# Kernel optimization log

Measured on AMD Instinct MI355X. Metric: run time of the kernel, lower is better.

Reference implementation:

```python
import jax, jax.numpy as jnp
import numpy as np

ALPHA = 0.2   # LeakyReLU negative slope
RATIO = 0.5   # blend ratio between attention and structural similarity
KHOP = 3      # k-hop structural similarity depth
NEG_BIG = -9e15


def _build_adj(edge, n):
    # edge: [N, D] int neighbor indices; adj[i, edge[i, d]] = 1
    rows = jnp.broadcast_to(jnp.arange(n)[:, None], edge.shape)
    return jnp.zeros((n, n), jnp.float32).at[rows, edge].set(1.0)


def _structural_similarity(adj, khop):
    # Sum of adjacency powers A + A^2 + ... + A^khop (k-hop reachability counts).
    s = adj
    p = adj
    for _ in range(khop - 1):
        p = p @ adj
        s = s + p
    return s


def _per_graph(atom, edge, W, a):
    n = atom.shape[0]
    adj = _build_adj(edge, n)
    structure = jax.nn.softmax(_structural_similarity(adj, KHOP), axis=1)
    h = atom @ W                                   # [N, F]
    f = h.shape[1]
    # a_input[i,j] = concat(h_i, h_j); a_input @ a == (h @ a1)_i + (h @ a2)_j
    src = h @ a[:f, 0]                             # [N]
    dst = h @ a[f:, 0]                             # [N]
    e = jax.nn.leaky_relu(src[:, None] + dst[None, :], ALPHA)  # [N, N]
    att = jnp.where(adj > 0, e, NEG_BIG)
    att = jax.nn.softmax(att, axis=1)
    blended = RATIO * att + (1.0 - RATIO) * structure
    return jax.nn.elu(blended @ h)                 # [N, F]


def setup_inputs() -> dict:
    key = jax.random.key(0)
    k1, k2, k3, k4 = jax.random.split(key, 4)
    B, N, D, F_IN, F_OUT = 16, 1024, 8, 128, 64
    atoms = jax.random.normal(k1, (B, N, F_IN), dtype=jnp.float32)
    edges = jax.random.randint(k2, (B, N, D), 0, N, dtype=jnp.int64)
    W = jax.random.normal(k3, (F_IN, F_OUT), dtype=jnp.float32) * 0.1
    a = jax.random.normal(k4, (2 * F_OUT, 1), dtype=jnp.float32) * 0.1
    return {"atoms": atoms, "edges": edges, "W": W, "a": a}


def reference(atoms, edges, W, a):
    return jax.vmap(_per_graph, in_axes=(0, 0, None, None))(atoms, edges, W, a)
```

## Files before the change

### kernel.cpp

```cpp
#include <hip/hip_runtime.h>

#define NN 1024
#define DG 8
#define FO 64
#define FI 128
#define LALPHA 0.2f
#define BR 16
#define SBS 257
#define MTS 1032

typedef __attribute__((ext_vector_type(8))) short bf16x8;
typedef __attribute__((ext_vector_type(4))) float f32x4;

static __device__ __forceinline__ unsigned short f2bf(float x) {
  union { float f; unsigned u; } v; v.f = x;
  unsigned r = v.u + 0x7FFFu + ((v.u >> 16) & 1u);
  return (unsigned short)(r >> 16);
}
static __device__ __forceinline__ float bf2f(unsigned short h) {
  union { unsigned u; float f; } v; v.u = ((unsigned)h) << 16;
  return v.f;
}

__global__ __launch_bounds__(256) void k_uniq(const int* __restrict__ edges,
                                              int* __restrict__ uniq, int nrows) {
  int r = blockIdx.x * 256 + threadIdx.x;
  if (r >= nrows) return;
  int e[DG];
#pragma unroll
  for (int s = 0; s < DG; s++) e[s] = edges[r * DG + s];
#pragma unroll
  for (int s = 0; s < DG; s++) {
    int v = e[s];
    bool dup = false;
#pragma unroll
    for (int q = 0; q < DG; q++)
      if (q < s && e[q] == v) dup = true;
    uniq[r * DG + s] = dup ? -1 : v;
  }
}

__global__ __launch_bounds__(256) void k_h(const float* __restrict__ atoms,
                                           const float* __restrict__ W,
                                           const float* __restrict__ a,
                                           ushort* __restrict__ hT,
                                           float* __restrict__ srcv,
                                           float* __restrict__ dstv) {
  __shared__ __align__(16) ushort Ahi[64 * 136], Alo[64 * 136];
  __shared__ __align__(16) ushort Whi[64 * 136], Wlo[64 * 136];
  __shared__ float al[2 * FO];
  const int t = threadIdx.x, b = blockIdx.x;

  const float4* at4 = (const float4*)(atoms + (size_t)b * 64 * FI);
#pragma unroll
  for (int q = 0; q < 8; q++) {
    int idx = t + 256 * q;
    float4 v = at4[idx];
    int row = idx >> 5, c4 = (idx & 31) * 4;
    ushort h0 = f2bf(v.x), h1 = f2bf(v.y), h2 = f2bf(v.z), h3 = f2bf(v.w);
    ushort l0 = f2bf(v.x - bf2f(h0)), l1 = f2bf(v.y - bf2f(h1));
    ushort l2_ = f2bf(v.z - bf2f(h2)), l3 = f2bf(v.w - bf2f(h3));
    union { uint2 v; ushort u[4]; } ph, pl;
    ph.u[0] = h0; ph.u[1] = h1; ph.u[2] = h2; ph.u[3] = h3;
    pl.u[0] = l0; pl.u[1] = l1; pl.u[2] = l2_; pl.u[3] = l3;
    *(uint2*)&Ahi[row * 136 + c4] = ph.v;
    *(uint2*)&Alo[row * 136 + c4] = pl.v;
  }
  const float4* w4 = (const float4*)W;
#pragma unroll
  for (int q = 0; q < 8; q++) {
    int idx = t + 256 * q;
    float4 v = w4[idx];
    int c = idx >> 4, f0 = (idx & 15) * 4;
    float vv[4] = {v.x, v.y, v.z, v.w};
#pragma unroll
    for (int e = 0; e < 4; e++) {
      ushort hi = f2bf(vv[e]);
      Whi[(f0 + e) * 136 + c] = hi;
      Wlo[(f0 + e) * 136 + c] = f2bf(vv[e] - bf2f(hi));
    }
  }
  if (t < 2 * FO) al[t] = a[t];
  __syncthreads();

  const int w = t >> 6, lane = t & 63, quad = lane >> 4, l16 = lane & 15;
  f32x4 acc[4] = {{0.f, 0.f, 0.f, 0.f}, {0.f, 0.f, 0.f, 0.f},
                  {0.f, 0.f, 0.f, 0.f}, {0.f, 0.f, 0.f, 0.f}};
#pragma unroll
  for (int kc = 0; kc < 4; kc++) {
    int ko = kc * 32 + quad * 8;
    bf16x8 ahi = *(const bf16x8*)&Ahi[(w * 16 + l16) * 136 + ko];
    bf16x8 alo = *(const bf16x8*)&Alo[(w * 16 + l16) * 136 + ko];
#pragma unroll
    for (int ct = 0; ct < 4; ct++) {
      bf16x8 bhi = *(const bf16x8*)&Whi[(ct * 16 + l16) * 136 + ko];
      bf16x8 blo = *(const bf16x8*)&Wlo[(ct * 16 + l16) * 136 + ko];
      acc[ct] = __builtin_amdgcn_mfma_f32_16x16x32_bf16(ahi, bhi, acc[ct], 0, 0, 0);
      acc[ct] = __builtin_amdgcn_mfma_f32_16x16x32_bf16(ahi, blo, acc[ct], 0, 0, 0);
      acc[ct] = __builtin_amdgcn_mfma_f32_16x16x32_bf16(alo, bhi, acc[ct], 0, 0, 0);
    }
  }

  const int g = b >> 4;
  float ps[4] = {0.f, 0.f, 0.f, 0.f}, pd[4] = {0.f, 0.f, 0.f, 0.f};
#pragma unroll
  for (int ct = 0; ct < 4; ct++) {
    int f = ct * 16 + l16;
    float as_ = al[f], ad_ = al[FO + f];
#pragma unroll
    for (int r = 0; r < 4; r++) {
      float v = acc[ct][r];
      int rb = b * 64 + w * 16 + quad * 4 + r;
      int n = rb & (NN - 1);
      hT[((size_t)g * FO + f) * NN + n] = f2bf(v);
      ps[r] += v * as_;
      pd[r] += v * ad_;
    }
  }
#pragma unroll
  for (int off = 8; off > 0; off >>= 1)
#pragma unroll
    for (int r = 0; r < 4; r++) {
      ps[r] += __shfl_xor(ps[r], off);
      pd[r] += __shfl_xor(pd[r], off);
    }
  if (l16 == 0) {
#pragma unroll
    for (int r = 0; r < 4; r++) {
      int rb = b * 64 + w * 16 + quad * 4 + r;
      srcv[rb] = ps[r];
      dstv[rb] = pd[r];
    }
  }
}

__global__ __launch_bounds__(256) void k_fused(const int* __restrict__ uniq,
                                               const float* __restrict__ srcv,
                                               const float* __restrict__ dstv,
                                               const ushort* __restrict__ hT,
                                               float* __restrict__ out) {
  __shared__ unsigned Sb[BR * SBS];
  __shared__ __align__(16) ushort Mt[BR * MTS];
  __shared__ int n1[BR][DG];
  __shared__ float attw[BR][DG];
  __shared__ float zl[BR][16];
  __shared__ float Zr[BR];

  const int t = threadIdx.x, b = blockIdx.x;
  const int g = b >> 6, rbase = (b & 63) * BR;
  const int* __restrict__ Ug = uniq + (size_t)g * NN * DG;

  for (int i = t; i < BR * SBS; i += 256) Sb[i] = 0u;
  if (t < BR * DG) n1[t >> 3][t & 7] = Ug[(rbase + (t >> 3)) * DG + (t & 7)];
  __syncthreads();

  if (t < 128) {
    int r = t >> 3, s = t & 7;
    int j = n1[r][s];
    if (j >= 0) {
      atomicAdd(&Sb[r * SBS + (j >> 2)], 1u << ((j & 3) * 8));
      int4 k0 = *(const int4*)(Ug + j * DG);
      int4 k1 = *(const int4*)(Ug + j * DG + 4);
      int kk[8] = {k0.x, k0.y, k0.z, k0.w, k1.x, k1.y, k1.z, k1.w};
#pragma unroll
      for (int e = 0; e < 8; e++)
        if (kk[e] >= 0) atomicAdd(&Sb[r * SBS + (kk[e] >> 2)], 1u << ((kk[e] & 3) * 8));
    }
  } else if (t < 128 + BR) {
    int r = t - 128;
    float si = srcv[g * NN + rbase + r];
    float ev[DG];
    float m = -1e30f;
#pragma unroll
    for (int s = 0; s < DG; s++) {
      int j = n1[r][s];
      if (j >= 0) {
        float x = si + dstv[g * NN + j];
        x = x > 0.f ? x : LALPHA * x;
        ev[s] = x;
        m = fmaxf(m, x);
      } else ev[s] = -1e30f;
    }
    float sm = 0.f;
#pragma unroll
    for (int s = 0; s < DG; s++) {
      float e = (n1[r][s] >= 0) ? __expf(ev[s] - m) : 0.f;
      ev[s] = e;
      sm += e;
    }
    float inv = 1.f / sm;
#pragma unroll
    for (int s = 0; s < DG; s++) attw[r][s] = ev[s] * inv;
  }
#pragma unroll
  for (int q = 0; q < 4; q++) {
    int idx = t + 256 * q;
    int r = idx >> 6, e = idx & 63;
    int j = n1[r][e >> 3];
    if (j >= 0) {
      int k = Ug[j * DG + (e & 7)];
      if (k >= 0) {
        int4 m0 = *(const int4*)(Ug + k * DG);
        int4 m1 = *(const int4*)(Ug + k * DG + 4);
        int ll[8] = {m0.x, m0.y, m0.z, m0.w, m1.x, m1.y, m1.z, m1.w};
#pragma unroll
        for (int e2 = 0; e2 < 8; e2++)
          if (ll[e2] >= 0) atomicAdd(&Sb[r * SBS + (ll[e2] >> 2)], 1u << ((ll[e2] & 3) * 8));
      }
    }
  }
  __syncthreads();

  {
    int r = t & 15, u = t >> 4;
    float zp = 0.f;
#pragma unroll
    for (int q = 0; q < 16; q++) {
      unsigned sv = Sb[r * SBS + u * 16 + q];
      zp += __expf((float)(sv & 255u)) + __expf((float)((sv >> 8) & 255u)) +
            __expf((float)((sv >> 16) & 255u)) + __expf((float)(sv >> 24));
    }
    zl[r][u] = zp;
  }
  __syncthreads();
  if (t < BR) {
    float s = 0.f;
#pragma unroll
    for (int u = 0; u < 16; u++) s += zl[t][u];
    Zr[t] = s;
  }
  __syncthreads();

  {
    int r = t & 15, u = t >> 4;
    float hzi = 0.5f / Zr[r];
#pragma unroll
    for (int q = 0; q < 8; q++) {
      unsigned s0 = Sb[r * SBS + u * 16 + 2 * q];
      unsigned s1 = Sb[r * SBS + u * 16 + 2 * q + 1];
      union { uint4 v; ushort us[8]; } pk;
      pk.us[0] = f2bf(hzi * __expf((float)(s0 & 255u)));
      pk.us[1] = f2bf(hzi * __expf((float)((s0 >> 8) & 255u)));
      pk.us[2] = f2bf(hzi * __expf((float)((s0 >> 16) & 255u)));
      pk.us[3] = f2bf(hzi * __expf((float)(s0 >> 24)));
      pk.us[4] = f2bf(hzi * __expf((float)(s1 & 255u)));
      pk.us[5] = f2bf(hzi * __expf((float)((s1 >> 8) & 255u)));
      pk.us[6] = f2bf(hzi * __expf((float)((s1 >> 16) & 255u)));
      pk.us[7] = f2bf(hzi * __expf((float)(s1 >> 24)));
      *(uint4*)&Mt[r * MTS + u * 64 + q * 8] = pk.v;
    }
  }
  __syncthreads();
  if (t < 128) {
    int r = t >> 3, s = t & 7;
    int j = n1[r][s];
    if (j >= 0) {
      int adr = r * MTS + j;
      Mt[adr] = f2bf(bf2f(Mt[adr]) + 0.5f * attw[r][s]);
    }
  }
  __syncthreads();

  const int w = t >> 6, lane = t & 63, quad = lane >> 4, l16 = lane & 15;
  const ushort* __restrict__ hrow = hT + ((size_t)g * FO + w * 16 + l16) * NN;
  f32x4 acc = {0.f, 0.f, 0.f, 0.f};
#pragma unroll 4
  for (int ks = 0; ks < NN; ks += 32) {
    bf16x8 af = *(const bf16x8*)&Mt[l16 * MTS + ks + quad * 8];
    bf16x8 bf = *(const bf16x8*)(hrow + ks + quad * 8);
    acc = __builtin_amdgcn_mfma_f32_16x16x32_bf16(af, bf, acc, 0, 0, 0);
  }
#pragma unroll
  for (int r = 0; r < 4; r++) {
    int row = rbase + quad * 4 + r;
    float v = acc[r];
    v = v > 0.f ? v : __expf(v) - 1.f;
    out[((size_t)(g * NN + row)) * FO + w * 16 + l16] = v;
  }
}

extern "C" void kernel_launch(void* const* d_in, const int* in_sizes, int n_in,
                              void* d_out, int out_size, void* d_ws, size_t ws_size,
                              hipStream_t stream) {
  const float* atoms = (const float*)d_in[0];
  const int* edges = (const int*)d_in[1];
  const float* W = (const float*)d_in[2];
  const float* a = (const float*)d_in[3];
  float* out = (float*)d_out;

  const int nrows = in_sizes[0] / FI;
  const int ngraph = nrows / NN;

  ushort* hT = (ushort*)d_ws;
  float* srcv = (float*)(hT + (size_t)ngraph * FO * NN);
  float* dstv = srcv + nrows;
  int* uniq = (int*)(dstv + nrows);

  k_uniq<<<(nrows + 255) / 256, 256, 0, stream>>>(edges, uniq, nrows);
  k_h<<<nrows / 64, 256, 0, stream>>>(atoms, W, a, hT, srcv, dstv);
  k_fused<<<ngraph * (NN / BR), 256, 0, stream>>>(uniq, srcv, dstv, hT, out);
}
```

Before: 99.54 us.

## Merge uniq and h kernels into one prep kernel; defer softmax normalization

Folds the edge-dedup kernel into the h-projection kernel, cutting one launch. The new kernel uses 16-row blocks and loads atoms and W straight from global memory into MFMA operands, with no LDS staging. In the fused kernel the structural softmax normalization moves to the epilogue, which removes a barrier and a reduction pass. The attention weights are pre-scaled by Z so the final single scale stays correct. Risks: uncoalesced strided W loads repeated across many more blocks, and bf16 rounding of unnormalized exp values, which can reach e^255 and overflow.

```diff
diff --git a/kernel.cpp b/kernel.cpp
--- a/kernel.cpp
+++ b/kernel.cpp
@@ -22,115 +22,94 @@
   return v.f;
 }
 
-__global__ __launch_bounds__(256) void k_uniq(const int* __restrict__ edges,
-                                              int* __restrict__ uniq, int nrows) {
-  int r = blockIdx.x * 256 + threadIdx.x;
-  if (r >= nrows) return;
-  int e[DG];
-#pragma unroll
-  for (int s = 0; s < DG; s++) e[s] = edges[r * DG + s];
-#pragma unroll
-  for (int s = 0; s < DG; s++) {
-    int v = e[s];
-    bool dup = false;
-#pragma unroll
-    for (int q = 0; q < DG; q++)
-      if (q < s && e[q] == v) dup = true;
-    uniq[r * DG + s] = dup ? -1 : v;
-  }
-}
-
-__global__ __launch_bounds__(256) void k_h(const float* __restrict__ atoms,
-                                           const float* __restrict__ W,
-                                           const float* __restrict__ a,
-                                           ushort* __restrict__ hT,
-                                           float* __restrict__ srcv,
-                                           float* __restrict__ dstv) {
-  __shared__ __align__(16) ushort Ahi[64 * 136], Alo[64 * 136];
-  __shared__ __align__(16) ushort Whi[64 * 136], Wlo[64 * 136];
-  __shared__ float al[2 * FO];
+__global__ __launch_bounds__(256) void k_prep(const float* __restrict__ atoms,
+                                              const float* __restrict__ W,
+                                              const float* __restrict__ a,
+                                              const int* __restrict__ edges,
+                                              int* __restrict__ uniq,
+                                              ushort* __restrict__ hT,
+                                              float* __restrict__ srcv,
+                                              float* __restrict__ dstv) {
+  __shared__ float sp[16], dp[16];
   const int t = threadIdx.x, b = blockIdx.x;
-
-  const float4* at4 = (const float4*)(atoms + (size_t)b * 64 * FI);
-#pragma unroll
-  for (int q = 0; q < 8; q++) {
-    int idx = t + 256 * q;
-    float4 v = at4[idx];
-    int row = idx >> 5, c4 = (idx & 31) * 4;
-    ushort h0 = f2bf(v.x), h1 = f2bf(v.y), h2 = f2bf(v.z), h3 = f2bf(v.w);
-    ushort l0 = f2bf(v.x - bf2f(h0)), l1 = f2bf(v.y - bf2f(h1));
-    ushort l2_ = f2bf(v.z - bf2f(h2)), l3 = f2bf(v.w - bf2f(h3));
-    union { uint2 v; ushort u[4]; } ph, pl;
-    ph.u[0] = h0; ph.u[1] = h1; ph.u[2] = h2; ph.u[3] = h3;
-    pl.u[0] = l0; pl.u[1] = l1; pl.u[2] = l2_; pl.u[3] = l3;
-    *(uint2*)&Ahi[row * 136 + c4] = ph.v;
-    *(uint2*)&Alo[row * 136 + c4] = pl.v;
-  }
-  const float4* w4 = (const float4*)W;
-#pragma unroll
-  for (int q = 0; q < 8; q++) {
-    int idx = t + 256 * q;
-    float4 v = w4[idx];
-    int c = idx >> 4, f0 = (idx & 15) * 4;
-    float vv[4] = {v.x, v.y, v.z, v.w};
-#pragma unroll
-    for (int e = 0; e < 4; e++) {
-      ushort hi = f2bf(vv[e]);
-      Whi[(f0 + e) * 136 + c] = hi;
-      Wlo[(f0 + e) * 136 + c] = f2bf(vv[e] - bf2f(hi));
-    }
-  }
-  if (t < 2 * FO) al[t] = a[t];
-  __syncthreads();
+  const int g = b >> 6;
+  const int rbase = b * 16;
+
+  if (t < 16) {
+    sp[t] = 0.f; dp[t] = 0.f;
+    const int rr = rbase + t;
+    int e[DG];
+#pragma unroll
+    for (int s = 0; s < DG; s++) e[s] = edges[rr * DG + s];
+#pragma unroll
+    for (int s = 0; s < DG; s++) {
+      int v = e[s];
+      bool dup = false;
+#pragma unroll
+      for (int q = 0; q < DG; q++)
+        if (q < s && e[q] == v) dup = true;
+      uniq[rr * DG + s] = dup ? -1 : v;
+    }
+  }
 
   const int w = t >> 6, lane = t & 63, quad = lane >> 4, l16 = lane & 15;
-  f32x4 acc[4] = {{0.f, 0.f, 0.f, 0.f}, {0.f, 0.f, 0.f, 0.f},
-                  {0.f, 0.f, 0.f, 0.f}, {0.f, 0.f, 0.f, 0.f}};
+  const float* __restrict__ Ar = atoms + (size_t)(rbase + l16) * FI;
+  const float* __restrict__ Wc = W + w * 16 + l16;
+  f32x4 acc = {0.f, 0.f, 0.f, 0.f};
 #pragma unroll
   for (int kc = 0; kc < 4; kc++) {
-    int ko = kc * 32 + quad * 8;
-    bf16x8 ahi = *(const bf16x8*)&Ahi[(w * 16 + l16) * 136 + ko];
-    bf16x8 alo = *(const bf16x8*)&Alo[(w * 16 + l16) * 136 + ko];
-#pragma unroll
-    for (int ct = 0; ct < 4; ct++) {
-      bf16x8 bhi = *(const bf16x8*)&Whi[(ct * 16 + l16) * 136 + ko];
-      bf16x8 blo = *(const bf16x8*)&Wlo[(ct * 16 + l16) * 136 + ko];
-      acc[ct] = __builtin_amdgcn_mfma_f32_16x16x32_bf16(ahi, bhi, acc[ct], 0, 0, 0);
-      acc[ct] = __builtin_amdgcn_mfma_f32_16x16x32_bf16(ahi, blo, acc[ct], 0, 0, 0);
-      acc[ct] = __builtin_amdgcn_mfma_f32_16x16x32_bf16(alo, bhi, acc[ct], 0, 0, 0);
-    }
-  }
-
-  const int g = b >> 4;
-  float ps[4] = {0.f, 0.f, 0.f, 0.f}, pd[4] = {0.f, 0.f, 0.f, 0.f};
-#pragma unroll
-  for (int ct = 0; ct < 4; ct++) {
-    int f = ct * 16 + l16;
-    float as_ = al[f], ad_ = al[FO + f];
-#pragma unroll
-    for (int r = 0; r < 4; r++) {
-      float v = acc[ct][r];
-      int rb = b * 64 + w * 16 + quad * 4 + r;
-      int n = rb & (NN - 1);
-      hT[((size_t)g * FO + f) * NN + n] = f2bf(v);
-      ps[r] += v * as_;
-      pd[r] += v * ad_;
-    }
-  }
-#pragma unroll
-  for (int off = 8; off > 0; off >>= 1)
+    const int k0 = kc * 32 + quad * 8;
+    float4 a0 = *(const float4*)(Ar + k0);
+    float4 a1 = *(const float4*)(Ar + k0 + 4);
+    float av[8] = {a0.x, a0.y, a0.z, a0.w, a1.x, a1.y, a1.z, a1.w};
+    float wv[8];
+#pragma unroll
+    for (int e = 0; e < 8; e++) wv[e] = Wc[(k0 + e) * FO];
+    bf16x8 ahi, alo, bhi, blo;
+#pragma unroll
+    for (int e = 0; e < 8; e++) {
+      ushort h = f2bf(av[e]);
+      ahi[e] = (short)h;
+      alo[e] = (short)f2bf(av[e] - bf2f(h));
+      ushort g2 = f2bf(wv[e]);
+      bhi[e] = (short)g2;
+      blo[e] = (short)f2bf(wv[e] - bf2f(g2));
+    }
+    acc = __builtin_amdgcn_mfma_f32_16x16x32_bf16(ahi, bhi, acc, 0, 0, 0);
+    acc = __builtin_amdgcn_mfma_f32_16x16x32_bf16(ahi, blo, acc, 0, 0, 0);
+    acc = __builtin_amdgcn_mfma_f32_16x16x32_bf16(alo, bhi, acc, 0, 0, 0);
+  }
+
+  const int f = w * 16 + l16;
+  const float as_ = a[f], ad_ = a[FO + f];
+  float ps[4], pd[4];
+#pragma unroll
+  for (int r = 0; r < 4; r++) {
+    float v = acc[r];
+    int rb = rbase + quad * 4 + r;
+    hT[((size_t)g * FO + f) * NN + (rb & (NN - 1))] = f2bf(v);
+    ps[r] = v * as_;
+    pd[r] = v * ad_;
+  }
+#pragma unroll
+  for (int off = 1; off < 16; off <<= 1)
 #pragma unroll
     for (int r = 0; r < 4; r++) {
       ps[r] += __shfl_xor(ps[r], off);
       pd[r] += __shfl_xor(pd[r], off);
     }
+  __syncthreads();
   if (l16 == 0) {
 #pragma unroll
     for (int r = 0; r < 4; r++) {
-      int rb = b * 64 + w * 16 + quad * 4 + r;
-      srcv[rb] = ps[r];
-      dstv[rb] = pd[r];
-    }
+      atomicAdd(&sp[quad * 4 + r], ps[r]);
+      atomicAdd(&dp[quad * 4 + r], pd[r]);
+    }
+  }
+  __syncthreads();
+  if (t < 16) {
+    srcv[rbase + t] = sp[t];
+    dstv[rbase + t] = dp[t];
   }
 }
 
@@ -212,51 +191,40 @@
   __syncthreads();
 
   {
-    int r = t & 15, u = t >> 4;
+    const int r = t & 15, u = t >> 4;
     float zp = 0.f;
-#pragma unroll
-    for (int q = 0; q < 16; q++) {
-      unsigned sv = Sb[r * SBS + u * 16 + q];
-      zp += __expf((float)(sv & 255u)) + __expf((float)((sv >> 8) & 255u)) +
-            __expf((float)((sv >> 16) & 255u)) + __expf((float)(sv >> 24));
-    }
-    zl[r][u] = zp;
-  }
-  __syncthreads();
-  if (t < BR) {
-    float s = 0.f;
-#pragma unroll
-    for (int u = 0; u < 16; u++) s += zl[t][u];
-    Zr[t] = s;
-  }
-  __syncthreads();
-
-  {
-    int r = t & 15, u = t >> 4;
-    float hzi = 0.5f / Zr[r];
 #pragma unroll
     for (int q = 0; q < 8; q++) {
       unsigned s0 = Sb[r * SBS + u * 16 + 2 * q];
       unsigned s1 = Sb[r * SBS + u * 16 + 2 * q + 1];
+      float e0 = __expf((float)(s0 & 255u));
+      float e1 = __expf((float)((s0 >> 8) & 255u));
+      float e2 = __expf((float)((s0 >> 16) & 255u));
+      float e3 = __expf((float)(s0 >> 24));
+      float e4 = __expf((float)(s1 & 255u));
+      float e5 = __expf((float)((s1 >> 8) & 255u));
+      float e6 = __expf((float)((s1 >> 16) & 255u));
+      float e7 = __expf((float)(s1 >> 24));
+      zp += (e0 + e1) + (e2 + e3) + (e4 + e5) + (e6 + e7);
       union { uint4 v; ushort us[8]; } pk;
-      pk.us[0] = f2bf(hzi * __expf((float)(s0 & 255u)));
-      pk.us[1] = f2bf(hzi * __expf((float)((s0 >> 8) & 255u)));
-      pk.us[2] = f2bf(hzi * __expf((float)((s0 >> 16) & 255u)));
-      pk.us[3] = f2bf(hzi * __expf((float)(s0 >> 24)));
-      pk.us[4] = f2bf(hzi * __expf((float)(s1 & 255u)));
-      pk.us[5] = f2bf(hzi * __expf((float)((s1 >> 8) & 255u)));
-      pk.us[6] = f2bf(hzi * __expf((float)((s1 >> 16) & 255u)));
-      pk.us[7] = f2bf(hzi * __expf((float)(s1 >> 24)));
+      pk.us[0] = f2bf(e0); pk.us[1] = f2bf(e1); pk.us[2] = f2bf(e2); pk.us[3] = f2bf(e3);
+      pk.us[4] = f2bf(e4); pk.us[5] = f2bf(e5); pk.us[6] = f2bf(e6); pk.us[7] = f2bf(e7);
       *(uint4*)&Mt[r * MTS + u * 64 + q * 8] = pk.v;
     }
-  }
-  __syncthreads();
+    zl[r][u] = zp;
+  }
+  __syncthreads();
+
   if (t < 128) {
-    int r = t >> 3, s = t & 7;
+    const int r = t >> 3, s = t & 7;
+    float z = 0.f;
+#pragma unroll
+    for (int u = 0; u < 16; u++) z += zl[r][u];
+    if (s == 0) Zr[r] = z;
     int j = n1[r][s];
     if (j >= 0) {
       int adr = r * MTS + j;
-      Mt[adr] = f2bf(bf2f(Mt[adr]) + 0.5f * attw[r][s]);
+      Mt[adr] = f2bf(bf2f(Mt[adr]) + attw[r][s] * z);
     }
   }
   __syncthreads();
@@ -264,7 +232,7 @@
   const int w = t >> 6, lane = t & 63, quad = lane >> 4, l16 = lane & 15;
   const ushort* __restrict__ hrow = hT + ((size_t)g * FO + w * 16 + l16) * NN;
   f32x4 acc = {0.f, 0.f, 0.f, 0.f};
-#pragma unroll 4
+#pragma unroll 8
   for (int ks = 0; ks < NN; ks += 32) {
     bf16x8 af = *(const bf16x8*)&Mt[l16 * MTS + ks + quad * 8];
     bf16x8 bf = *(const bf16x8*)(hrow + ks + quad * 8);
@@ -272,10 +240,10 @@
   }
 #pragma unroll
   for (int r = 0; r < 4; r++) {
-    int row = rbase + quad * 4 + r;
-    float v = acc[r];
+    int rl = quad * 4 + r;
+    float v = acc[r] * (0.5f / Zr[rl]);
     v = v > 0.f ? v : __expf(v) - 1.f;
-    out[((size_t)(g * NN + row)) * FO + w * 16 + l16] = v;
+    out[((size_t)(g * NN + rbase + rl)) * FO + w * 16 + l16] = v;
   }
 }
 
@@ -296,7 +264,6 @@
   float* dstv = srcv + nrows;
   int* uniq = (int*)(dstv + nrows);
 
-  k_uniq<<<(nrows + 255) / 256, 256, 0, stream>>>(edges, uniq, nrows);
-  k_h<<<nrows / 64, 256, 0, stream>>>(atoms, W, a, hT, srcv, dstv);
+  k_prep<<<nrows / 16, 256, 0, stream>>>(atoms, W, a, edges, uniq, hT, srcv, dstv);
   k_fused<<<ngraph * (NN / BR), 256, 0, stream>>>(uniq, srcv, dstv, hT, out);
 }
```

Result: no change. 101.5 us (+1.9%).
